# Kernel optimization log

Measured on AMD Instinct MI355X. Metric: run time of the kernel, lower is better.

The kernel has to match this reference:

```python
import jax, jax.numpy as jnp
import numpy as np

N_NODES = 50000
N_EDGES = 600000
D_IN = 128
D_OUT = 128


def mean_propagate(x, edge_index, num_nodes):
    # edge_index[0] = source nodes, edge_index[1] = destination nodes
    src, dst = edge_index[0], edge_index[1]
    gathered = x[src]                                   # [E, D]
    summed = jax.ops.segment_sum(gathered, dst, num_segments=num_nodes)  # [N, D]
    deg = jax.ops.segment_sum(jnp.ones((edge_index.shape[1],), dtype=x.dtype), dst,
                              num_segments=num_nodes)   # [N]
    deg = jnp.maximum(deg, 1.0)
    return summed / deg[:, None]


def setup_inputs() -> dict:
    key = jax.random.key(0)
    k1, k2, k3 = jax.random.split(key, 3)
    x = jax.random.normal(k1, (N_NODES, D_IN), dtype=jnp.float32)
    edge_index = jax.random.randint(k2, (2, N_EDGES), 0, N_NODES, dtype=jnp.int64)
    # nn.Linear(in_channels*3, out_channels): weight [out, 3*in], bias [out]
    W = jax.random.normal(k3, (D_OUT, 3 * D_IN), dtype=jnp.float32) / np.sqrt(3 * D_IN)
    b = jnp.zeros((D_OUT,), dtype=jnp.float32)
    return {"x": x, "edge_index": edge_index, "W": W, "b": b}


def reference(x, edge_index, W, b):
    n = x.shape[0]
    hop1 = mean_propagate(x, edge_index, n)
    hop2 = mean_propagate(hop1, edge_index, n)
    feats = jnp.concatenate([x, hop1, hop2], axis=-1)   # [N, 3*D]
    return feats @ W.T + b                              # [N, D_OUT]
```

## Files before the change

kernel.cpp:

```cpp
#include <hip/hip_runtime.h>

#define N_NODES 50000
#define N_EDGES 600000
#define D 128
#define K3 (3 * D)
#define NB_G 1563
#define NREP 8

typedef __attribute__((ext_vector_type(8))) short short8;
typedef __attribute__((ext_vector_type(4))) float floatx4;
typedef __attribute__((ext_vector_type(8))) unsigned short ushort8;

static __device__ __forceinline__ unsigned short f2bf(float f) {
    unsigned u = __float_as_uint(f);
    u += 0x7fff + ((u >> 16) & 1);
    return (unsigned short)(u >> 16);
}
static __device__ __forceinline__ float bf2f(unsigned short s) {
    return __uint_as_float(((unsigned)s) << 16);
}
static __device__ __forceinline__ unsigned pack2(float a, float b) {
    return (unsigned)f2bf(a) | ((unsigned)f2bf(b) << 16);
}

__global__ __launch_bounds__(256) void zero_kernel(int* __restrict__ counts8) {
    int i = blockIdx.x * 256 + threadIdx.x;
    if (i < NREP * N_NODES) counts8[i] = 0;
}

__global__ __launch_bounds__(256) void prep_kernel(const float* __restrict__ x,
                                                   const float* __restrict__ W,
                                                   const int* __restrict__ dst,
                                                   unsigned short* __restrict__ xb,
                                                   unsigned short* __restrict__ Wr,
                                                   int* __restrict__ counts8) {
    const int stride = gridDim.x * 256;
    const int t0 = blockIdx.x * 256 + threadIdx.x;
    for (int u = t0; u < N_EDGES / 4; u += stride) {
        int4 d4 = ((const int4*)dst)[u];
        int* base = counts8 + (u & 7) * N_NODES;
        atomicAdd(base + d4.x, 1);
        atomicAdd(base + d4.y, 1);
        atomicAdd(base + d4.z, 1);
        atomicAdd(base + d4.w, 1);
    }
    for (unsigned t = t0; t < (unsigned)N_NODES * 16; t += stride) {
        unsigned n = t >> 4;
        unsigned c = (t & 15u) << 3;
        const float4 v0 = *(const float4*)(x + (size_t)n * D + c);
        const float4 v1 = *(const float4*)(x + (size_t)n * D + c + 4);
        ushort8 o;
        o[0] = f2bf(v0.x); o[1] = f2bf(v0.y); o[2] = f2bf(v0.z); o[3] = f2bf(v0.w);
        o[4] = f2bf(v1.x); o[5] = f2bf(v1.y); o[6] = f2bf(v1.z); o[7] = f2bf(v1.w);
        *(ushort8*)(xb + (size_t)n * D + c) = o;
    }
    for (unsigned id = t0; id < 24u * 4u * 64u; id += stride) {
        unsigned T = id >> 8;
        unsigned ks = (id >> 6) & 3u;
        unsigned lane = id & 63u;
        unsigned c = lane & 15u;
        unsigned q = lane >> 4;
        unsigned row = (T & 7u) * 16u + c;
        unsigned k = (T >> 3) * 128u + ks * 32u + q * 8u;
        const float4 v0 = *(const float4*)(W + (size_t)row * K3 + k);
        const float4 v1 = *(const float4*)(W + (size_t)row * K3 + k + 4);
        ushort8 o;
        o[0] = f2bf(v0.x); o[1] = f2bf(v0.y); o[2] = f2bf(v0.z); o[3] = f2bf(v0.w);
        o[4] = f2bf(v1.x); o[5] = f2bf(v1.y); o[6] = f2bf(v1.z); o[7] = f2bf(v1.w);
        *(ushort8*)(Wr + (size_t)id * 8) = o;
    }
}

#define LDSROW 104
__global__ __launch_bounds__(256) void gemm_kernel(const unsigned short* __restrict__ xb,
                                                   const unsigned short* __restrict__ Wr,
                                                   const float* __restrict__ bias,
                                                   unsigned short* __restrict__ z) {
    __shared__ unsigned short lds[4 * 32 * LDSROW];
    const int blk = blockIdx.x;
    const int tid = threadIdx.x;
    const int wave = tid >> 6;
    const int lane = tid & 63;
    const int col = lane & 15;
    const int quad = lane >> 4;
    const int mbase = blk * 32;
    const int T0 = wave * 6;

    int r0 = mbase + col;
    int r1 = mbase + 16 + col;
    if (r0 >= N_NODES) r0 = N_NODES - 1;
    if (r1 >= N_NODES) r1 = N_NODES - 1;
    const unsigned short* ap0 = xb + (size_t)r0 * D + quad * 8;
    const unsigned short* ap1 = xb + (size_t)r1 * D + quad * 8;

    floatx4 acc0[6], acc1[6];
#pragma unroll
    for (int t = 0; t < 6; ++t) {
        acc0[t] = (floatx4){0.f, 0.f, 0.f, 0.f};
        acc1[t] = (floatx4){0.f, 0.f, 0.f, 0.f};
    }

#pragma unroll
    for (int ks = 0; ks < 4; ++ks) {
        short8 a0 = *(const short8*)(ap0 + ks * 32);
        short8 a1 = *(const short8*)(ap1 + ks * 32);
#pragma unroll
        for (int t = 0; t < 6; ++t) {
            short8 bb = *(const short8*)(Wr + (size_t)(((T0 + t) * 4 + ks) * 64 + lane) * 8);
            acc0[t] = __builtin_amdgcn_mfma_f32_16x16x32_bf16(bb, a0, acc0[t], 0, 0, 0);
            acc1[t] = __builtin_amdgcn_mfma_f32_16x16x32_bf16(bb, a1, acc1[t], 0, 0, 0);
        }
    }

    unsigned short* wlds = lds + wave * 32 * LDSROW;
#pragma unroll
    for (int t = 0; t < 6; ++t) {
        int T = T0 + t;
        float4 bq = (float4){0.f, 0.f, 0.f, 0.f};
        if (T < 8) bq = *(const float4*)(bias + T * 16 + quad * 4);
        uint2 p;
        p.x = pack2(acc0[t][0] + bq.x, acc0[t][1] + bq.y);
        p.y = pack2(acc0[t][2] + bq.z, acc0[t][3] + bq.w);
        *(uint2*)(wlds + col * LDSROW + t * 16 + quad * 4) = p;
        uint2 q2;
        q2.x = pack2(acc1[t][0] + bq.x, acc1[t][1] + bq.y);
        q2.y = pack2(acc1[t][2] + bq.z, acc1[t][3] + bq.w);
        *(uint2*)(wlds + (col + 16) * LDSROW + t * 16 + quad * 4) = q2;
    }
    __syncthreads();
#pragma unroll
    for (int it = 0; it < 6; ++it) {
        int id = it * 64 + lane;
        int row = id / 12;
        int ch = id - row * 12;
        int node = mbase + row;
        ushort8 v = *(const ushort8*)(wlds + row * LDSROW + ch * 8);
        if (node < N_NODES)
            *(ushort8*)(z + (size_t)node * K3 + T0 * 16 + ch * 8) = v;
    }
}

__global__ __launch_bounds__(256) void bsum_kernel(const int* __restrict__ counts8,
                                                   int* __restrict__ ctot,
                                                   int* __restrict__ bsum) {
    __shared__ int wsum[4];
    int tid = threadIdx.x;
    int i = blockIdx.x * 256 + tid;
    int v = 0;
    if (i < N_NODES) {
#pragma unroll
        for (int r = 0; r < NREP; ++r) v += counts8[r * N_NODES + i];
        ctot[i] = v;
    }
#pragma unroll
    for (int d = 32; d >= 1; d >>= 1) v += __shfl_xor(v, d);
    if ((tid & 63) == 0) wsum[tid >> 6] = v;
    __syncthreads();
    if (tid == 0) bsum[blockIdx.x] = wsum[0] + wsum[1] + wsum[2] + wsum[3];
}

__global__ __launch_bounds__(256) void scan_bsum_kernel(const int* __restrict__ bsum,
                                                        int* __restrict__ bexcl,
                                                        int* __restrict__ off, int nb) {
    __shared__ int wsum[4];
    int tid = threadIdx.x;
    int lane = tid & 63, wid = tid >> 6;
    int v = (tid < nb) ? bsum[tid] : 0;
    int x = v;
#pragma unroll
    for (int d = 1; d < 64; d <<= 1) {
        int u = __shfl_up(x, d);
        if (lane >= d) x += u;
    }
    if (lane == 63) wsum[wid] = x;
    __syncthreads();
    int prefix = 0;
    for (int w = 0; w < wid; ++w) prefix += wsum[w];
    if (tid < nb) bexcl[tid] = prefix + x - v;
    if (tid == 0) off[N_NODES] = N_EDGES;
}

__global__ __launch_bounds__(256) void scan_final_kernel(const int* __restrict__ ctot,
                                                         const int* __restrict__ counts8,
                                                         const int* __restrict__ bexcl,
                                                         int* __restrict__ off,
                                                         int* __restrict__ cursor8) {
    __shared__ int wsum[4];
    int tid = threadIdx.x;
    int lane = tid & 63, wid = tid >> 6;
    int i = blockIdx.x * 256 + tid;
    int v = (i < N_NODES) ? ctot[i] : 0;
    int x = v;
#pragma unroll
    for (int d = 1; d < 64; d <<= 1) {
        int u = __shfl_up(x, d);
        if (lane >= d) x += u;
    }
    if (lane == 63) wsum[wid] = x;
    __syncthreads();
    int prefix = 0;
    for (int w = 0; w < wid; ++w) prefix += wsum[w];
    if (i < N_NODES) {
        int excl = bexcl[blockIdx.x] + prefix + x - v;
        off[i] = excl;
        int run = excl;
#pragma unroll
        for (int r = 0; r < NREP; ++r) {
            cursor8[r * N_NODES + i] = run;
            run += counts8[r * N_NODES + i];
        }
    }
}

__global__ __launch_bounds__(256) void fill_kernel(const int* __restrict__ src,
                                                   const int* __restrict__ dst,
                                                   int* __restrict__ cursor8,
                                                   int* __restrict__ csr_src) {
    int u = blockIdx.x * 256 + threadIdx.x;
    if (u < N_EDGES / 4) {
        int4 s4 = ((const int4*)src)[u];
        int4 d4 = ((const int4*)dst)[u];
        int* cbase = cursor8 + (u & 7) * N_NODES;
        csr_src[atomicAdd(cbase + d4.x, 1)] = s4.x;
        csr_src[atomicAdd(cbase + d4.y, 1)] = s4.y;
        csr_src[atomicAdd(cbase + d4.z, 1)] = s4.z;
        csr_src[atomicAdd(cbase + d4.w, 1)] = s4.w;
    }
}

__global__ __launch_bounds__(256) void gather1_kernel(const unsigned short* __restrict__ z,
                                                      const int* __restrict__ off,
                                                      const int* __restrict__ csr_src,
                                                      unsigned short* __restrict__ tb) {
    unsigned n = (blockIdx.x * 256 + threadIdx.x) >> 6;
    if (n >= N_NODES) return;
    const int lane = threadIdx.x & 63;
    const int s = lane >> 4;
    const unsigned c = (lane & 15u) << 3;
    const unsigned short* fin = z + 256 + c;
    const int2 ee = *(const int2*)(off + n);
    const int e0 = ee.x, e1 = ee.y;
    float acc[8] = {0.f, 0.f, 0.f, 0.f, 0.f, 0.f, 0.f, 0.f};
    for (int base = (e0 & ~3) + s * 4; base < e1; base += 16) {
        int4 idx = *(const int4*)(csr_src + base);
        float m0 = (base >= e0) ? 1.f : 0.f;
        float m1 = (base + 1 >= e0 && base + 1 < e1) ? 1.f : 0.f;
        float m2 = (base + 2 >= e0 && base + 2 < e1) ? 1.f : 0.f;
        float m3 = (base + 3 >= e0 && base + 3 < e1) ? 1.f : 0.f;
        int s0 = min(max(idx.x, 0), N_NODES - 1);
        int s1 = min(max(idx.y, 0), N_NODES - 1);
        int s2 = min(max(idx.z, 0), N_NODES - 1);
        int s3 = min(max(idx.w, 0), N_NODES - 1);
        ushort8 v0 = *(const ushort8*)(fin + (size_t)s0 * K3);
        ushort8 v1 = *(const ushort8*)(fin + (size_t)s1 * K3);
        ushort8 v2 = *(const ushort8*)(fin + (size_t)s2 * K3);
        ushort8 v3 = *(const ushort8*)(fin + (size_t)s3 * K3);
#pragma unroll
        for (int j = 0; j < 8; ++j)
            acc[j] += (m0 * bf2f(v0[j]) + m1 * bf2f(v1[j])) +
                      (m2 * bf2f(v2[j]) + m3 * bf2f(v3[j]));
    }
#pragma unroll
    for (int j = 0; j < 8; ++j) {
        acc[j] += __shfl_xor(acc[j], 16);
        acc[j] += __shfl_xor(acc[j], 32);
    }
    if (s == 0) {
        float inv = 1.0f / fmaxf((float)(e1 - e0), 1.0f);
        ushort8 za = *(const ushort8*)(z + (size_t)n * K3 + 128 + c);
        ushort8 o;
#pragma unroll
        for (int j = 0; j < 8; ++j) o[j] = f2bf(bf2f(za[j]) + acc[j] * inv);
        *(ushort8*)(tb + (size_t)n * D + c) = o;
    }
}

__global__ __launch_bounds__(256) void gather2_kernel(const unsigned short* __restrict__ z,
                                                      const unsigned short* __restrict__ tb,
                                                      const int* __restrict__ off,
                                                      const int* __restrict__ csr_src,
                                                      float* __restrict__ out) {
    unsigned n = (blockIdx.x * 256 + threadIdx.x) >> 6;
    if (n >= N_NODES) return;
    const int lane = threadIdx.x & 63;
    const int s = lane >> 4;
    const unsigned c = (lane & 15u) << 3;
    const unsigned short* fin = tb + c;
    const int2 ee = *(const int2*)(off + n);
    const int e0 = ee.x, e1 = ee.y;
    float acc[8] = {0.f, 0.f, 0.f, 0.f, 0.f, 0.f, 0.f, 0.f};
    for (int base = (e0 & ~3) + s * 4; base < e1; base += 16) {
        int4 idx = *(const int4*)(csr_src + base);
        float m0 = (base >= e0) ? 1.f : 0.f;
        float m1 = (base + 1 >= e0 && base + 1 < e1) ? 1.f : 0.f;
        float m2 = (base + 2 >= e0 && base + 2 < e1) ? 1.f : 0.f;
        float m3 = (base + 3 >= e0 && base + 3 < e1) ? 1.f : 0.f;
        int s0 = min(max(idx.x, 0), N_NODES - 1);
        int s1 = min(max(idx.y, 0), N_NODES - 1);
        int s2 = min(max(idx.z, 0), N_NODES - 1);
        int s3 = min(max(idx.w, 0), N_NODES - 1);
        ushort8 v0 = *(const ushort8*)(fin + (size_t)s0 * D);
        ushort8 v1 = *(const ushort8*)(fin + (size_t)s1 * D);
        ushort8 v2 = *(const ushort8*)(fin + (size_t)s2 * D);
        ushort8 v3 = *(const ushort8*)(fin + (size_t)s3 * D);
#pragma unroll
        for (int j = 0; j < 8; ++j)
            acc[j] += (m0 * bf2f(v0[j]) + m1 * bf2f(v1[j])) +
                      (m2 * bf2f(v2[j]) + m3 * bf2f(v3[j]));
    }
#pragma unroll
    for (int j = 0; j < 8; ++j) {
        acc[j] += __shfl_xor(acc[j], 16);
        acc[j] += __shfl_xor(acc[j], 32);
    }
    if (s == 0) {
        float inv = 1.0f / fmaxf((float)(e1 - e0), 1.0f);
        ushort8 za = *(const ushort8*)(z + (size_t)n * K3 + c);
        float4 q0, q1;
        q0.x = bf2f(za[0]) + acc[0] * inv;
        q0.y = bf2f(za[1]) + acc[1] * inv;
        q0.z = bf2f(za[2]) + acc[2] * inv;
        q0.w = bf2f(za[3]) + acc[3] * inv;
        q1.x = bf2f(za[4]) + acc[4] * inv;
        q1.y = bf2f(za[5]) + acc[5] * inv;
        q1.z = bf2f(za[6]) + acc[6] * inv;
        q1.w = bf2f(za[7]) + acc[7] * inv;
        *(float4*)(out + (size_t)n * D + c) = q0;
        *(float4*)(out + (size_t)n * D + c + 4) = q1;
    }
}

extern "C" void kernel_launch(void* const* d_in, const int* in_sizes, int n_in,
                              void* d_out, int out_size, void* d_ws, size_t ws_size,
                              hipStream_t stream) {
    const float* x = (const float*)d_in[0];
    const int* ei = (const int*)d_in[1];
    const float* W = (const float*)d_in[2];
    const float* b = (const float*)d_in[3];
    float* out = (float*)d_out;
    const int* src = ei;
    const int* dst = ei + N_EDGES;

    unsigned short* xb = (unsigned short*)d_ws;
    unsigned short* z = xb + (size_t)N_NODES * D;
    unsigned short* tb = z + (size_t)N_NODES * K3;
    unsigned short* Wr = tb + (size_t)N_NODES * D;
    int* counts8 = (int*)(Wr + 6144 * 8);
    int* ctot = counts8 + NREP * N_NODES;
    int* bsum = ctot + N_NODES;
    int* bexcl = bsum + 256;
    int* off = bexcl + 256;
    int* cursor8 = off + (N_NODES + 4);
    int* csr_src = cursor8 + NREP * N_NODES;

    const int NB = (N_NODES + 255) / 256;

    zero_kernel<<<(NREP * N_NODES + 255) / 256, 256, 0, stream>>>(counts8);
    prep_kernel<<<800, 256, 0, stream>>>(x, W, dst, xb, Wr, counts8);
    gemm_kernel<<<NB_G, 256, 0, stream>>>(xb, Wr, b, z);
    bsum_kernel<<<NB, 256, 0, stream>>>(counts8, ctot, bsum);
    scan_bsum_kernel<<<1, 256, 0, stream>>>(bsum, bexcl, off, NB);
    scan_final_kernel<<<NB, 256, 0, stream>>>(ctot, counts8, bexcl, off, cursor8);
    fill_kernel<<<(N_EDGES / 4 + 255) / 256, 256, 0, stream>>>(src, dst, cursor8, csr_src);

    const int ggrid = (N_NODES * 64 + 255) / 256;
    gather1_kernel<<<ggrid, 256, 0, stream>>>(z, off, csr_src, tb);
    gather2_kernel<<<ggrid, 256, 0, stream>>>(z, tb, off, csr_src, out);
}
```

Baseline: 213.1 us.

## Fuse all stages into one cooperative persistent kernel with grid syncs

Replaces nine separate kernel launches with a single cooperative kernel of 768 persistent blocks that run the stages back to back, separated by grid.sync. The degree-counting atomics overlap with the GEMM by splitting blocks between the two tasks. The aim is to remove launch gaps and tail effects between the many small kernels. In exchange, each grid barrier has a cost, the gather phases run with fixed persistent parallelism instead of one wave per node launch, and the multi-kernel path is kept as a fallback if the cooperative launch fails.

```diff
diff --git a/kernel.cpp b/kernel.cpp
--- a/kernel.cpp
+++ b/kernel.cpp
@@ -1,4 +1,7 @@
 #include <hip/hip_runtime.h>
+#include <hip/hip_cooperative_groups.h>
+
+namespace cg = cooperative_groups;
 
 #define N_NODES 50000
 #define N_EDGES 600000
@@ -6,6 +9,10 @@
 #define K3 (3 * D)
 #define NB_G 1563
 #define NREP 8
+#define NB 196
+#define NBLK 768
+#define GEMM_SPLIT 600
+#define LDSROW 104
 
 typedef __attribute__((ext_vector_type(8))) short short8;
 typedef __attribute__((ext_vector_type(4))) float floatx4;
@@ -21,6 +28,288 @@
 }
 static __device__ __forceinline__ unsigned pack2(float a, float b) {
     return (unsigned)f2bf(a) | ((unsigned)f2bf(b) << 16);
+}
+
+__global__ __launch_bounds__(256, 4) void mega_kernel(
+    const float* __restrict__ x, const float* __restrict__ W,
+    const int* __restrict__ src, const int* __restrict__ dst,
+    const float* __restrict__ bias, float* __restrict__ out,
+    unsigned short* __restrict__ xb, unsigned short* __restrict__ z,
+    unsigned short* __restrict__ tb, unsigned short* __restrict__ Wr,
+    int* __restrict__ counts8, int* __restrict__ ctot,
+    int* __restrict__ bsum, int* __restrict__ bexcl,
+    int* __restrict__ off, int* __restrict__ cursor8,
+    int* __restrict__ csr_src) {
+    cg::grid_group grid = cg::this_grid();
+    __shared__ unsigned short lds[4 * 32 * LDSROW];
+    __shared__ int wsum[4];
+    const int tid = threadIdx.x;
+    const int gtid = blockIdx.x * 256 + tid;
+    const int gstride = NBLK * 256;
+    const int wave = tid >> 6;
+    const int lane = tid & 63;
+    const int col = lane & 15;
+    const int quad = lane >> 4;
+
+    for (int i = gtid; i < NREP * N_NODES; i += gstride) counts8[i] = 0;
+    for (unsigned t = gtid; t < (unsigned)N_NODES * 16; t += gstride) {
+        unsigned n = t >> 4;
+        unsigned c = (t & 15u) << 3;
+        const float4 v0 = *(const float4*)(x + (size_t)n * D + c);
+        const float4 v1 = *(const float4*)(x + (size_t)n * D + c + 4);
+        ushort8 o;
+        o[0] = f2bf(v0.x); o[1] = f2bf(v0.y); o[2] = f2bf(v0.z); o[3] = f2bf(v0.w);
+        o[4] = f2bf(v1.x); o[5] = f2bf(v1.y); o[6] = f2bf(v1.z); o[7] = f2bf(v1.w);
+        *(ushort8*)(xb + (size_t)n * D + c) = o;
+    }
+    for (unsigned id = gtid; id < 24u * 4u * 64u; id += gstride) {
+        unsigned T = id >> 8;
+        unsigned ks = (id >> 6) & 3u;
+        unsigned ln = id & 63u;
+        unsigned c = ln & 15u;
+        unsigned q = ln >> 4;
+        unsigned row = (T & 7u) * 16u + c;
+        unsigned k = (T >> 3) * 128u + ks * 32u + q * 8u;
+        const float4 v0 = *(const float4*)(W + (size_t)row * K3 + k);
+        const float4 v1 = *(const float4*)(W + (size_t)row * K3 + k + 4);
+        ushort8 o;
+        o[0] = f2bf(v0.x); o[1] = f2bf(v0.y); o[2] = f2bf(v0.z); o[3] = f2bf(v0.w);
+        o[4] = f2bf(v1.x); o[5] = f2bf(v1.y); o[6] = f2bf(v1.z); o[7] = f2bf(v1.w);
+        *(ushort8*)(Wr + (size_t)id * 8) = o;
+    }
+    grid.sync();
+
+    if (blockIdx.x < GEMM_SPLIT) {
+        for (int blk = blockIdx.x; blk < NB_G; blk += GEMM_SPLIT) {
+            const int mbase = blk * 32;
+            const int T0 = wave * 6;
+            int r0 = mbase + col;
+            int r1 = mbase + 16 + col;
+            if (r0 >= N_NODES) r0 = N_NODES - 1;
+            if (r1 >= N_NODES) r1 = N_NODES - 1;
+            const unsigned short* ap0 = xb + (size_t)r0 * D + quad * 8;
+            const unsigned short* ap1 = xb + (size_t)r1 * D + quad * 8;
+            floatx4 acc0[6], acc1[6];
+#pragma unroll
+            for (int t = 0; t < 6; ++t) {
+                acc0[t] = (floatx4){0.f, 0.f, 0.f, 0.f};
+                acc1[t] = (floatx4){0.f, 0.f, 0.f, 0.f};
+            }
+#pragma unroll
+            for (int ks = 0; ks < 4; ++ks) {
+                short8 a0 = *(const short8*)(ap0 + ks * 32);
+                short8 a1 = *(const short8*)(ap1 + ks * 32);
+#pragma unroll
+                for (int t = 0; t < 6; ++t) {
+                    short8 bb = *(const short8*)(Wr + (size_t)(((T0 + t) * 4 + ks) * 64 + lane) * 8);
+                    acc0[t] = __builtin_amdgcn_mfma_f32_16x16x32_bf16(bb, a0, acc0[t], 0, 0, 0);
+                    acc1[t] = __builtin_amdgcn_mfma_f32_16x16x32_bf16(bb, a1, acc1[t], 0, 0, 0);
+                }
+            }
+            unsigned short* wlds = lds + wave * 32 * LDSROW;
+#pragma unroll
+            for (int t = 0; t < 6; ++t) {
+                int T = T0 + t;
+                float4 bq = (float4){0.f, 0.f, 0.f, 0.f};
+                if (T < 8) bq = *(const float4*)(bias + T * 16 + quad * 4);
+                uint2 p;
+                p.x = pack2(acc0[t][0] + bq.x, acc0[t][1] + bq.y);
+                p.y = pack2(acc0[t][2] + bq.z, acc0[t][3] + bq.w);
+                *(uint2*)(wlds + col * LDSROW + t * 16 + quad * 4) = p;
+                uint2 q2;
+                q2.x = pack2(acc1[t][0] + bq.x, acc1[t][1] + bq.y);
+                q2.y = pack2(acc1[t][2] + bq.z, acc1[t][3] + bq.w);
+                *(uint2*)(wlds + (col + 16) * LDSROW + t * 16 + quad * 4) = q2;
+            }
+            __syncthreads();
+#pragma unroll
+            for (int it = 0; it < 6; ++it) {
+                int id = it * 64 + lane;
+                int row = id / 12;
+                int ch = id - row * 12;
+                int node = mbase + row;
+                ushort8 v = *(const ushort8*)(wlds + row * LDSROW + ch * 8);
+                if (node < N_NODES)
+                    *(ushort8*)(z + (size_t)node * K3 + T0 * 16 + ch * 8) = v;
+            }
+            __syncthreads();
+        }
+    } else {
+        for (int u = (blockIdx.x - GEMM_SPLIT) * 256 + tid; u < N_EDGES / 4;
+             u += (NBLK - GEMM_SPLIT) * 256) {
+            int4 d4 = ((const int4*)dst)[u];
+            int* base = counts8 + (u & 7) * N_NODES;
+            atomicAdd(base + d4.x, 1);
+            atomicAdd(base + d4.y, 1);
+            atomicAdd(base + d4.z, 1);
+            atomicAdd(base + d4.w, 1);
+        }
+    }
+    grid.sync();
+
+    if (blockIdx.x < NB) {
+        int i = blockIdx.x * 256 + tid;
+        int v = 0;
+        if (i < N_NODES) {
+#pragma unroll
+            for (int r = 0; r < NREP; ++r) v += counts8[r * N_NODES + i];
+            ctot[i] = v;
+        }
+#pragma unroll
+        for (int d = 32; d >= 1; d >>= 1) v += __shfl_xor(v, d);
+        if ((tid & 63) == 0) wsum[tid >> 6] = v;
+        __syncthreads();
+        if (tid == 0) bsum[blockIdx.x] = wsum[0] + wsum[1] + wsum[2] + wsum[3];
+    }
+    grid.sync();
+
+    if (blockIdx.x == 0) {
+        int v = (tid < NB) ? bsum[tid] : 0;
+        int xs = v;
+#pragma unroll
+        for (int d = 1; d < 64; d <<= 1) {
+            int u = __shfl_up(xs, d);
+            if (lane >= d) xs += u;
+        }
+        if (lane == 63) wsum[wave] = xs;
+        __syncthreads();
+        int prefix = 0;
+        for (int w = 0; w < wave; ++w) prefix += wsum[w];
+        if (tid < NB) bexcl[tid] = prefix + xs - v;
+        if (tid == 0) off[N_NODES] = N_EDGES;
+    }
+    grid.sync();
+
+    if (blockIdx.x < NB) {
+        int i = blockIdx.x * 256 + tid;
+        int v = (i < N_NODES) ? ctot[i] : 0;
+        int xs = v;
+#pragma unroll
+        for (int d = 1; d < 64; d <<= 1) {
+            int u = __shfl_up(xs, d);
+            if (lane >= d) xs += u;
+        }
+        if (lane == 63) wsum[wave] = xs;
+        __syncthreads();
+        int prefix = 0;
+        for (int w = 0; w < wave; ++w) prefix += wsum[w];
+        if (i < N_NODES) {
+            int excl = bexcl[blockIdx.x] + prefix + xs - v;
+            off[i] = excl;
+            int run = excl;
+#pragma unroll
+            for (int r = 0; r < NREP; ++r) {
+                cursor8[r * N_NODES + i] = run;
+                run += counts8[r * N_NODES + i];
+            }
+        }
+    }
+    grid.sync();
+
+    for (int u = gtid; u < N_EDGES / 4; u += gstride) {
+        int4 s4 = ((const int4*)src)[u];
+        int4 d4 = ((const int4*)dst)[u];
+        int* cbase = cursor8 + (u & 7) * N_NODES;
+        csr_src[atomicAdd(cbase + d4.x, 1)] = s4.x;
+        csr_src[atomicAdd(cbase + d4.y, 1)] = s4.y;
+        csr_src[atomicAdd(cbase + d4.z, 1)] = s4.z;
+        csr_src[atomicAdd(cbase + d4.w, 1)] = s4.w;
+    }
+    grid.sync();
+
+    {
+        const int s = quad;
+        const unsigned c = ((unsigned)col) << 3;
+        const unsigned short* fin = z + 256 + c;
+        for (int n = blockIdx.x * 4 + wave; n < N_NODES; n += NBLK * 4) {
+            const int2 ee = *(const int2*)(off + n);
+            const int e0 = ee.x, e1 = ee.y;
+            float acc[8] = {0.f, 0.f, 0.f, 0.f, 0.f, 0.f, 0.f, 0.f};
+            for (int base = (e0 & ~3) + s * 4; base < e1; base += 16) {
+                int4 idx = *(const int4*)(csr_src + base);
+                float m0 = (base >= e0) ? 1.f : 0.f;
+                float m1 = (base + 1 >= e0 && base + 1 < e1) ? 1.f : 0.f;
+                float m2 = (base + 2 >= e0 && base + 2 < e1) ? 1.f : 0.f;
+                float m3 = (base + 3 >= e0 && base + 3 < e1) ? 1.f : 0.f;
+                int s0 = min(max(idx.x, 0), N_NODES - 1);
+                int s1 = min(max(idx.y, 0), N_NODES - 1);
+                int s2 = min(max(idx.z, 0), N_NODES - 1);
+                int s3 = min(max(idx.w, 0), N_NODES - 1);
+                ushort8 v0 = *(const ushort8*)(fin + (size_t)s0 * K3);
+                ushort8 v1 = *(const ushort8*)(fin + (size_t)s1 * K3);
+                ushort8 v2 = *(const ushort8*)(fin + (size_t)s2 * K3);
+                ushort8 v3 = *(const ushort8*)(fin + (size_t)s3 * K3);
+#pragma unroll
+                for (int j = 0; j < 8; ++j)
+                    acc[j] += (m0 * bf2f(v0[j]) + m1 * bf2f(v1[j])) +
+                              (m2 * bf2f(v2[j]) + m3 * bf2f(v3[j]));
+            }
+#pragma unroll
+            for (int j = 0; j < 8; ++j) {
+                acc[j] += __shfl_xor(acc[j], 16);
+                acc[j] += __shfl_xor(acc[j], 32);
+            }
+            if (s == 0) {
+                float inv = 1.0f / fmaxf((float)(e1 - e0), 1.0f);
+                ushort8 za = *(const ushort8*)(z + (size_t)n * K3 + 128 + c);
+                ushort8 o;
+#pragma unroll
+                for (int j = 0; j < 8; ++j) o[j] = f2bf(bf2f(za[j]) + acc[j] * inv);
+                *(ushort8*)(tb + (size_t)n * D + c) = o;
+            }
+        }
+    }
+    grid.sync();
+
+    {
+        const int s = quad;
+        const unsigned c = ((unsigned)col) << 3;
+        const unsigned short* fin = tb + c;
+        for (int n = blockIdx.x * 4 + wave; n < N_NODES; n += NBLK * 4) {
+            const int2 ee = *(const int2*)(off + n);
+            const int e0 = ee.x, e1 = ee.y;
+            float acc[8] = {0.f, 0.f, 0.f, 0.f, 0.f, 0.f, 0.f, 0.f};
+            for (int base = (e0 & ~3) + s * 4; base < e1; base += 16) {
+                int4 idx = *(const int4*)(csr_src + base);
+                float m0 = (base >= e0) ? 1.f : 0.f;
+                float m1 = (base + 1 >= e0 && base + 1 < e1) ? 1.f : 0.f;
+                float m2 = (base + 2 >= e0 && base + 2 < e1) ? 1.f : 0.f;
+                float m3 = (base + 3 >= e0 && base + 3 < e1) ? 1.f : 0.f;
+                int s0 = min(max(idx.x, 0), N_NODES - 1);
+                int s1 = min(max(idx.y, 0), N_NODES - 1);
+                int s2 = min(max(idx.z, 0), N_NODES - 1);
+                int s3 = min(max(idx.w, 0), N_NODES - 1);
+                ushort8 v0 = *(const ushort8*)(fin + (size_t)s0 * D);
+                ushort8 v1 = *(const ushort8*)(fin + (size_t)s1 * D);
+                ushort8 v2 = *(const ushort8*)(fin + (size_t)s2 * D);
+                ushort8 v3 = *(const ushort8*)(fin + (size_t)s3 * D);
+#pragma unroll
+                for (int j = 0; j < 8; ++j)
+                    acc[j] += (m0 * bf2f(v0[j]) + m1 * bf2f(v1[j])) +
+                              (m2 * bf2f(v2[j]) + m3 * bf2f(v3[j]));
+            }
+#pragma unroll
+            for (int j = 0; j < 8; ++j) {
+                acc[j] += __shfl_xor(acc[j], 16);
+                acc[j] += __shfl_xor(acc[j], 32);
+            }
+            if (s == 0) {
+                float inv = 1.0f / fmaxf((float)(e1 - e0), 1.0f);
+                ushort8 za = *(const ushort8*)(z + (size_t)n * K3 + c);
+                float4 q0, q1;
+                q0.x = bf2f(za[0]) + acc[0] * inv;
+                q0.y = bf2f(za[1]) + acc[1] * inv;
+                q0.z = bf2f(za[2]) + acc[2] * inv;
+                q0.w = bf2f(za[3]) + acc[3] * inv;
+                q1.x = bf2f(za[4]) + acc[4] * inv;
+                q1.y = bf2f(za[5]) + acc[5] * inv;
+                q1.z = bf2f(za[6]) + acc[6] * inv;
+                q1.w = bf2f(za[7]) + acc[7] * inv;
+                *(float4*)(out + (size_t)n * D + c) = q0;
+                *(float4*)(out + (size_t)n * D + c + 4) = q1;
+            }
+        }
+    }
 }
 
 __global__ __launch_bounds__(256) void zero_kernel(int* __restrict__ counts8) {
@@ -71,7 +360,6 @@
     }
 }
 
-#define LDSROW 104
 __global__ __launch_bounds__(256) void gemm_kernel(const unsigned short* __restrict__ xb,
                                                    const unsigned short* __restrict__ Wr,
                                                    const float* __restrict__ bias,
@@ -85,21 +373,18 @@
     const int quad = lane >> 4;
     const int mbase = blk * 32;
     const int T0 = wave * 6;
-
     int r0 = mbase + col;
     int r1 = mbase + 16 + col;
     if (r0 >= N_NODES) r0 = N_NODES - 1;
     if (r1 >= N_NODES) r1 = N_NODES - 1;
     const unsigned short* ap0 = xb + (size_t)r0 * D + quad * 8;
     const unsigned short* ap1 = xb + (size_t)r1 * D + quad * 8;
-
     floatx4 acc0[6], acc1[6];
 #pragma unroll
     for (int t = 0; t < 6; ++t) {
         acc0[t] = (floatx4){0.f, 0.f, 0.f, 0.f};
         acc1[t] = (floatx4){0.f, 0.f, 0.f, 0.f};
     }
-
 #pragma unroll
     for (int ks = 0; ks < 4; ++ks) {
         short8 a0 = *(const short8*)(ap0 + ks * 32);
@@ -111,7 +396,6 @@
             acc1[t] = __builtin_amdgcn_mfma_f32_16x16x32_bf16(bb, a1, acc1[t], 0, 0, 0);
         }
     }
-
     unsigned short* wlds = lds + wave * 32 * LDSROW;
 #pragma unroll
     for (int t = 0; t < 6; ++t) {
@@ -347,23 +631,29 @@
     unsigned short* Wr = tb + (size_t)N_NODES * D;
     int* counts8 = (int*)(Wr + 6144 * 8);
     int* ctot = counts8 + NREP * N_NODES;
-    int* bsum = ctot + N_NODES;
-    int* bexcl = bsum + 256;
-    int* off = bexcl + 256;
-    int* cursor8 = off + (N_NODES + 4);
-    int* csr_src = cursor8 + NREP * N_NODES;
-
-    const int NB = (N_NODES + 255) / 256;
-
-    zero_kernel<<<(NREP * N_NODES + 255) / 256, 256, 0, stream>>>(counts8);
-    prep_kernel<<<800, 256, 0, stream>>>(x, W, dst, xb, Wr, counts8);
-    gemm_kernel<<<NB_G, 256, 0, stream>>>(xb, Wr, b, z);
-    bsum_kernel<<<NB, 256, 0, stream>>>(counts8, ctot, bsum);
-    scan_bsum_kernel<<<1, 256, 0, stream>>>(bsum, bexcl, off, NB);
-    scan_final_kernel<<<NB, 256, 0, stream>>>(ctot, counts8, bexcl, off, cursor8);
-    fill_kernel<<<(N_EDGES / 4 + 255) / 256, 256, 0, stream>>>(src, dst, cursor8, csr_src);
-
-    const int ggrid = (N_NODES * 64 + 255) / 256;
-    gather1_kernel<<<ggrid, 256, 0, stream>>>(z, off, csr_src, tb);
-    gather2_kernel<<<ggrid, 256, 0, stream>>>(z, tb, off, csr_src, out);
-}
+    int* bsumv = ctot + N_NODES;
+    int* bexclv = bsumv + 256;
+    int* offv = bexclv + 256;
+    int* cursor8v = offv + (N_NODES + 4);
+    int* csrv = cursor8v + NREP * N_NODES;
+
+    void* kargs[] = {(void*)&x,      (void*)&W,     (void*)&src,    (void*)&dst,
+                     (void*)&b,      (void*)&out,   (void*)&xb,     (void*)&z,
+                     (void*)&tb,     (void*)&Wr,    (void*)&counts8, (void*)&ctot,
+                     (void*)&bsumv,  (void*)&bexclv, (void*)&offv,  (void*)&cursor8v,
+                     (void*)&csrv};
+    hipError_t err = hipLaunchCooperativeKernel((void*)mega_kernel, dim3(NBLK), dim3(256),
+                                                kargs, 0, stream);
+    if (err != hipSuccess) {
+        zero_kernel<<<(NREP * N_NODES + 255) / 256, 256, 0, stream>>>(counts8);
+        prep_kernel<<<800, 256, 0, stream>>>(x, W, dst, xb, Wr, counts8);
+        gemm_kernel<<<NB_G, 256, 0, stream>>>(xb, Wr, b, z);
+        bsum_kernel<<<NB, 256, 0, stream>>>(counts8, ctot, bsumv);
+        scan_bsum_kernel<<<1, 256, 0, stream>>>(bsumv, bexclv, offv, NB);
+        scan_final_kernel<<<NB, 256, 0, stream>>>(ctot, counts8, bexclv, offv, cursor8v);
+        fill_kernel<<<(N_EDGES / 4 + 255) / 256, 256, 0, stream>>>(src, dst, cursor8v, csrv);
+        const int ggrid = (N_NODES * 64 + 255) / 256;
+        gather1_kernel<<<ggrid, 256, 0, stream>>>(z, offv, csrv, tb);
+        gather2_kernel<<<ggrid, 256, 0, stream>>>(z, tb, offv, csrv, out);
+    }
+}
```

New measurement: 851.8 us. 300% more time.
